# Kernel optimization log

Hardware: AMD Instinct MI355X
Metric: run time of the kernel (lower is better)

Reference implementation:

```python
import jax, jax.numpy as jnp
import numpy as np

B, N, C, H, W = 4, 5, 64, 100, 252  # N agents per sample (uniform record_len)


def setup_inputs() -> dict:
    key = jax.random.key(0)
    k1, k2, k3 = jax.random.split(key, 3)
    x = jax.random.normal(k1, (B * N, C, H, W), dtype=jnp.float32)
    rm = jax.random.normal(k2, (B * N, 2, H, W), dtype=jnp.float32)
    record_len = jnp.full((B,), N, dtype=jnp.int32)
    # normalized 2x3 affines (identity + small perturbation), shape (B, L, L, 2, 3)
    eye = jnp.broadcast_to(jnp.array([[1.0, 0.0, 0.0], [0.0, 1.0, 0.0]], jnp.float32), (B, N, N, 2, 3))
    pairwise_t_matrix = eye + 0.05 * jax.random.normal(k3, (B, N, N, 2, 3), dtype=jnp.float32)
    return {"x": x, "rm": rm, "record_len": record_len, "pairwise_t_matrix": pairwise_t_matrix}


def _warp_affine(feats, theta):
    # feats: (N, C, H, W), theta: (N, 2, 3). torch affine_grid + grid_sample,
    # bilinear, zeros padding, align_corners=False.
    xs = (2.0 * jnp.arange(W, dtype=jnp.float32) + 1.0) / W - 1.0
    ys = (2.0 * jnp.arange(H, dtype=jnp.float32) + 1.0) / H - 1.0
    gy, gx = jnp.meshgrid(ys, xs, indexing="ij")           # (H, W)
    base = jnp.stack([gx, gy, jnp.ones_like(gx)], axis=-1)  # (H, W, 3)
    coords = jnp.einsum("nij,hwj->nhwi", theta, base)       # (N, H, W, 2) normalized
    ix = ((coords[..., 0] + 1.0) * W - 1.0) * 0.5            # input pixel coords
    iy = ((coords[..., 1] + 1.0) * H - 1.0) * 0.5
    x0 = jnp.floor(ix); y0 = jnp.floor(iy)
    x1 = x0 + 1.0;      y1 = y0 + 1.0
    wx1 = ix - x0; wx0 = 1.0 - wx1
    wy1 = iy - y0; wy0 = 1.0 - wy1

    def gather(xi, yi):
        valid = (xi >= 0) & (xi <= W - 1) & (yi >= 0) & (yi <= H - 1)
        xc = jnp.clip(xi, 0, W - 1).astype(jnp.int32)
        yc = jnp.clip(yi, 0, H - 1).astype(jnp.int32)
        v = jax.vmap(lambda f, yy, xx: f[:, yy, xx])(feats, yc, xc)  # (N, C, H, W)
        return v * valid[:, None, :, :].astype(feats.dtype)

    out = (gather(x0, y0) * (wx0 * wy0)[:, None]
         + gather(x1, y0) * (wx1 * wy0)[:, None]
         + gather(x0, y1) * (wx0 * wy1)[:, None]
         + gather(x1, y1) * (wx1 * wy1)[:, None])
    return out  # (N, C, H, W)


def reference(x, rm, record_len, pairwise_t_matrix):
    # Where2commFusion, single-scale, MAX agg, communication disabled.
    # regroup: uniform record_len -> reshape (B, N, C, H, W)
    xr = x.reshape(B, N, C, H, W)
    theta = pairwise_t_matrix[:, 0, :, :, :]  # t_matrix[0, :N] per batch: (B, N, 2, 3)
    warped = jax.vmap(_warp_affine)(xr, theta)  # (B, N, C, H, W)
    x_fuse = jnp.max(warped, axis=1)            # (B, C, H, W)
    communication_rates = jnp.zeros((), dtype=jnp.float32)
    return (x_fuse, communication_rates)
```

## Files before the change

kernel.cpp:

```cpp
#include <hip/hip_runtime.h>
#include <math.h>

#define BB 4
#define NN 5
#define CC_DIM 64
#define HH 100
#define WW 252
#define HW (HH * WW)
#define CPT 8
#define NCHUNK (CC_DIM / CPT)

__global__ __launch_bounds__(256) void where2comm_fuse_kernel(
    const float* __restrict__ x,
    const float* __restrict__ ptm,
    float* __restrict__ out)
{
    const int idx = blockIdx.x * blockDim.x + threadIdx.x;
    const int total = BB * NCHUNK * HH * WW;
    if (idx >= total) {
        return;
    }

    int w = idx % WW;
    int t = idx / WW;
    int h = t % HH;
    t /= HH;
    int cc = t % NCHUNK;
    int b = t / NCHUNK;

    const float gx = (2.0f * (float)w + 1.0f) / (float)WW - 1.0f;
    const float gy = (2.0f * (float)h + 1.0f) / (float)HH - 1.0f;

    float acc[CPT];
#pragma unroll
    for (int c = 0; c < CPT; ++c) acc[c] = -INFINITY;

    const float* th_b = ptm + (size_t)b * (NN * NN * 6);

#pragma unroll
    for (int n = 0; n < NN; ++n) {
        const float t00 = th_b[n * 6 + 0];
        const float t01 = th_b[n * 6 + 1];
        const float t02 = th_b[n * 6 + 2];
        const float t10 = th_b[n * 6 + 3];
        const float t11 = th_b[n * 6 + 4];
        const float t12 = th_b[n * 6 + 5];

        const float cx = t00 * gx + t01 * gy + t02;
        const float cy = t10 * gx + t11 * gy + t12;

        const float ix = ((cx + 1.0f) * (float)WW - 1.0f) * 0.5f;
        const float iy = ((cy + 1.0f) * (float)HH - 1.0f) * 0.5f;

        const float x0f = floorf(ix);
        const float y0f = floorf(iy);
        const float x1f = x0f + 1.0f;
        const float y1f = y0f + 1.0f;

        const float wx1 = ix - x0f;
        const float wx0 = 1.0f - wx1;
        const float wy1 = iy - y0f;
        const float wy0 = 1.0f - wy1;

        const float mx0 = (x0f >= 0.0f && x0f <= (float)(WW - 1)) ? 1.0f : 0.0f;
        const float mx1 = (x1f >= 0.0f && x1f <= (float)(WW - 1)) ? 1.0f : 0.0f;
        const float my0 = (y0f >= 0.0f && y0f <= (float)(HH - 1)) ? 1.0f : 0.0f;
        const float my1 = (y1f >= 0.0f && y1f <= (float)(HH - 1)) ? 1.0f : 0.0f;

        const int xi0 = (int)fminf(fmaxf(x0f, 0.0f), (float)(WW - 1));
        const int xi1 = (int)fminf(fmaxf(x1f, 0.0f), (float)(WW - 1));
        const int yi0 = (int)fminf(fmaxf(y0f, 0.0f), (float)(HH - 1));
        const int yi1 = (int)fminf(fmaxf(y1f, 0.0f), (float)(HH - 1));

        const float e00 = wx0 * wy0 * mx0 * my0;
        const float e10 = wx1 * wy0 * mx1 * my0;
        const float e01 = wx0 * wy1 * mx0 * my1;
        const float e11 = wx1 * wy1 * mx1 * my1;

        const int o00 = yi0 * WW + xi0;
        const int o10 = yi0 * WW + xi1;
        const int o01 = yi1 * WW + xi0;
        const int o11 = yi1 * WW + xi1;

        const float* p = x + ((size_t)(b * NN + n) * CC_DIM + cc * CPT) * HW;

        float v00[CPT], v10[CPT], v01[CPT], v11[CPT];
#pragma unroll
        for (int c = 0; c < CPT; ++c) {
            const float* pc = p + (size_t)c * HW;
            v00[c] = pc[o00];
            v10[c] = pc[o10];
            v01[c] = pc[o01];
            v11[c] = pc[o11];
        }

#pragma unroll
        for (int c = 0; c < CPT; ++c) {
            float v = v00[c] * e00;
            v = fmaf(v10[c], e10, v);
            v = fmaf(v01[c], e01, v);
            v = fmaf(v11[c], e11, v);
            acc[c] = fmaxf(acc[c], v);
        }
    }

#pragma unroll
    for (int c = 0; c < CPT; ++c) {
        out[(((size_t)b * CC_DIM + cc * CPT + c) * HH + h) * WW + w] = acc[c];
    }

    if (idx == 0) {
        out[(size_t)BB * CC_DIM * HW] = 0.0f;
    }
}

extern "C" void kernel_launch(void* const* d_in, const int* in_sizes, int n_in,
                              void* d_out, int out_size, void* d_ws, size_t ws_size,
                              hipStream_t stream) {
    const float* x = (const float*)d_in[0];
    const float* ptm = (const float*)d_in[3];
    float* out = (float*)d_out;

    const int total = BB * NCHUNK * HH * WW;
    const int block = 256;
    const int grid = (total + block - 1) / block;
    where2comm_fuse_kernel<<<grid, block, 0, stream>>>(x, ptm, out);
}
```

Measured before the change: 58.02 us.

## Compute two output rows per thread and reuse shared bilinear source rows

Each thread now produces two adjacent output rows and loads each bilinear 2x2 window as two 8-byte row pairs from a clamped base, with clamping folded into the weights. When the second row's window matches or is one row below the first, the already-loaded source row is reused instead of reloaded. This aims to cut gather load count and per-pixel index math. It adds register pressure, divergent reuse branches and possibly unaligned vector loads.

```diff
diff --git a/kernel.cpp b/kernel.cpp
--- a/kernel.cpp
+++ b/kernel.cpp
@@ -9,6 +9,7 @@
 #define HW (HH * WW)
 #define CPT 8
 #define NCHUNK (CC_DIM / CPT)
+#define HP (HH / 2)
 
 __global__ __launch_bounds__(256) void where2comm_fuse_kernel(
     const float* __restrict__ x,
@@ -16,26 +17,26 @@
     float* __restrict__ out)
 {
     const int idx = blockIdx.x * blockDim.x + threadIdx.x;
-    const int total = BB * NCHUNK * HH * WW;
-    if (idx >= total) {
-        return;
-    }
 
     int w = idx % WW;
     int t = idx / WW;
-    int h = t % HH;
-    t /= HH;
+    int hp = t % HP;
+    t /= HP;
     int cc = t % NCHUNK;
     int b = t / NCHUNK;
 
+    const int h0 = 2 * hp;
+    const int h1 = h0 + 1;
+
     const float gx = (2.0f * (float)w + 1.0f) / (float)WW - 1.0f;
-    const float gy = (2.0f * (float)h + 1.0f) / (float)HH - 1.0f;
-
-    float acc[CPT];
-#pragma unroll
-    for (int c = 0; c < CPT; ++c) acc[c] = -INFINITY;
+    const float gy0 = (2.0f * (float)h0 + 1.0f) / (float)HH - 1.0f;
+    const float gy1 = (2.0f * (float)h1 + 1.0f) / (float)HH - 1.0f;
 
     const float* th_b = ptm + (size_t)b * (NN * NN * 6);
+
+    float acc0[CPT], acc1[CPT];
+#pragma unroll
+    for (int c = 0; c < CPT; ++c) { acc0[c] = -INFINITY; acc1[c] = -INFINITY; }
 
 #pragma unroll
     for (int n = 0; n < NN; ++n) {
@@ -46,67 +47,115 @@
         const float t11 = th_b[n * 6 + 4];
         const float t12 = th_b[n * 6 + 5];
 
-        const float cx = t00 * gx + t01 * gy + t02;
-        const float cy = t10 * gx + t11 * gy + t12;
+        int clA, rlA, clB, rlB;
+        float gA00, gA01, gA10, gA11, gB00, gB01, gB10, gB11;
 
-        const float ix = ((cx + 1.0f) * (float)WW - 1.0f) * 0.5f;
-        const float iy = ((cy + 1.0f) * (float)HH - 1.0f) * 0.5f;
+#define GEOM(GY, CL, RL, G00, G01, G10, G11)                                   \
+        {                                                                      \
+            const float cx = t00 * gx + t01 * (GY) + t02;                      \
+            const float cy = t10 * gx + t11 * (GY) + t12;                      \
+            const float ix = ((cx + 1.0f) * (float)WW - 1.0f) * 0.5f;          \
+            const float iy = ((cy + 1.0f) * (float)HH - 1.0f) * 0.5f;          \
+            const float x0f = floorf(ix);                                      \
+            const float y0f = floorf(iy);                                      \
+            const float x1f = x0f + 1.0f;                                      \
+            const float y1f = y0f + 1.0f;                                      \
+            const float wx1 = ix - x0f;                                        \
+            const float wx0 = 1.0f - wx1;                                      \
+            const float wy1 = iy - y0f;                                        \
+            const float wy0 = 1.0f - wy1;                                      \
+            const float mx0 = (x0f >= 0.0f && x0f <= (float)(WW - 1)) ? 1.0f : 0.0f; \
+            const float mx1 = (x1f >= 0.0f && x1f <= (float)(WW - 1)) ? 1.0f : 0.0f; \
+            const float my0 = (y0f >= 0.0f && y0f <= (float)(HH - 1)) ? 1.0f : 0.0f; \
+            const float my1 = (y1f >= 0.0f && y1f <= (float)(HH - 1)) ? 1.0f : 0.0f; \
+            const float e00 = wx0 * wy0 * mx0 * my0;                           \
+            const float e10 = wx1 * wy0 * mx1 * my0;                           \
+            const float e01 = wx0 * wy1 * mx0 * my1;                           \
+            const float e11 = wx1 * wy1 * mx1 * my1;                           \
+            const int xi0 = (int)fminf(fmaxf(x0f, 0.0f), (float)(WW - 1));     \
+            const int xi1 = (int)fminf(fmaxf(x1f, 0.0f), (float)(WW - 1));     \
+            const int yi0 = (int)fminf(fmaxf(y0f, 0.0f), (float)(HH - 1));     \
+            const int yi1 = (int)fminf(fmaxf(y1f, 0.0f), (float)(HH - 1));     \
+            CL = (int)fminf(fmaxf(x0f, 0.0f), (float)(WW - 2));                \
+            RL = (int)fminf(fmaxf(y0f, 0.0f), (float)(HH - 2));                \
+            const float sx0 = (float)(xi0 - CL);                               \
+            const float sx1 = (float)(xi1 - CL);                               \
+            const float sy0 = (float)(yi0 - RL);                               \
+            const float sy1 = (float)(yi1 - RL);                               \
+            const float nx0 = 1.0f - sx0, nx1 = 1.0f - sx1;                    \
+            const float ny0 = 1.0f - sy0, ny1 = 1.0f - sy1;                    \
+            G00 = e00 * nx0 * ny0 + e10 * nx1 * ny0 + e01 * nx0 * ny1 + e11 * nx1 * ny1; \
+            G01 = e00 * sx0 * ny0 + e10 * sx1 * ny0 + e01 * sx0 * ny1 + e11 * sx1 * ny1; \
+            G10 = e00 * nx0 * sy0 + e10 * nx1 * sy0 + e01 * nx0 * sy1 + e11 * nx1 * sy1; \
+            G11 = e00 * sx0 * sy0 + e10 * sx1 * sy0 + e01 * sx0 * sy1 + e11 * sx1 * sy1; \
+        }
 
-        const float x0f = floorf(ix);
-        const float y0f = floorf(iy);
-        const float x1f = x0f + 1.0f;
-        const float y1f = y0f + 1.0f;
+        GEOM(gy0, clA, rlA, gA00, gA01, gA10, gA11)
+        GEOM(gy1, clB, rlB, gB00, gB01, gB10, gB11)
+#undef GEOM
 
-        const float wx1 = ix - x0f;
-        const float wx0 = 1.0f - wx1;
-        const float wy1 = iy - y0f;
-        const float wy0 = 1.0f - wy1;
+        const float* plane = x + ((size_t)(b * NN + n) * CC_DIM + cc * CPT) * HW;
+        const int offA = rlA * WW + clA;
+        const int offB = rlB * WW + clB;
 
-        const float mx0 = (x0f >= 0.0f && x0f <= (float)(WW - 1)) ? 1.0f : 0.0f;
-        const float mx1 = (x1f >= 0.0f && x1f <= (float)(WW - 1)) ? 1.0f : 0.0f;
-        const float my0 = (y0f >= 0.0f && y0f <= (float)(HH - 1)) ? 1.0f : 0.0f;
-        const float my1 = (y1f >= 0.0f && y1f <= (float)(HH - 1)) ? 1.0f : 0.0f;
-
-        const int xi0 = (int)fminf(fmaxf(x0f, 0.0f), (float)(WW - 1));
-        const int xi1 = (int)fminf(fmaxf(x1f, 0.0f), (float)(WW - 1));
-        const int yi0 = (int)fminf(fmaxf(y0f, 0.0f), (float)(HH - 1));
-        const int yi1 = (int)fminf(fmaxf(y1f, 0.0f), (float)(HH - 1));
-
-        const float e00 = wx0 * wy0 * mx0 * my0;
-        const float e10 = wx1 * wy0 * mx1 * my0;
-        const float e01 = wx0 * wy1 * mx0 * my1;
-        const float e11 = wx1 * wy1 * mx1 * my1;
-
-        const int o00 = yi0 * WW + xi0;
-        const int o10 = yi0 * WW + xi1;
-        const int o01 = yi1 * WW + xi0;
-        const int o11 = yi1 * WW + xi1;
-
-        const float* p = x + ((size_t)(b * NN + n) * CC_DIM + cc * CPT) * HW;
-
-        float v00[CPT], v10[CPT], v01[CPT], v11[CPT];
+        float L0[CPT][2], L1[CPT][2];
 #pragma unroll
         for (int c = 0; c < CPT; ++c) {
-            const float* pc = p + (size_t)c * HW;
-            v00[c] = pc[o00];
-            v10[c] = pc[o10];
-            v01[c] = pc[o01];
-            v11[c] = pc[o11];
+            const float* pc = plane + (size_t)c * HW + offA;
+            __builtin_memcpy(&L0[c][0], pc, 8);
+            __builtin_memcpy(&L1[c][0], pc + WW, 8);
         }
 
 #pragma unroll
         for (int c = 0; c < CPT; ++c) {
-            float v = v00[c] * e00;
-            v = fmaf(v10[c], e10, v);
-            v = fmaf(v01[c], e01, v);
-            v = fmaf(v11[c], e11, v);
-            acc[c] = fmaxf(acc[c], v);
+            float v = L0[c][0] * gA00;
+            v = fmaf(L0[c][1], gA01, v);
+            v = fmaf(L1[c][0], gA10, v);
+            v = fmaf(L1[c][1], gA11, v);
+            acc0[c] = fmaxf(acc0[c], v);
+        }
+
+        const bool sameCol = (clB == clA);
+        const bool reuse0 = sameCol && (rlB == rlA);
+        const bool reuse1 = sameCol && (rlB == rlA + 1);
+
+        float P[CPT][2], Q[CPT][2];
+        if (reuse0) {
+#pragma unroll
+            for (int c = 0; c < CPT; ++c) {
+                P[c][0] = L0[c][0]; P[c][1] = L0[c][1];
+                Q[c][0] = L1[c][0]; Q[c][1] = L1[c][1];
+            }
+        } else if (reuse1) {
+#pragma unroll
+            for (int c = 0; c < CPT; ++c) {
+                P[c][0] = L1[c][0]; P[c][1] = L1[c][1];
+                __builtin_memcpy(&Q[c][0], plane + (size_t)c * HW + offB + WW, 8);
+            }
+        } else {
+#pragma unroll
+            for (int c = 0; c < CPT; ++c) {
+                const float* pc = plane + (size_t)c * HW + offB;
+                __builtin_memcpy(&P[c][0], pc, 8);
+                __builtin_memcpy(&Q[c][0], pc + WW, 8);
+            }
+        }
+
+#pragma unroll
+        for (int c = 0; c < CPT; ++c) {
+            float v = P[c][0] * gB00;
+            v = fmaf(P[c][1], gB01, v);
+            v = fmaf(Q[c][0], gB10, v);
+            v = fmaf(Q[c][1], gB11, v);
+            acc1[c] = fmaxf(acc1[c], v);
         }
     }
 
 #pragma unroll
     for (int c = 0; c < CPT; ++c) {
-        out[(((size_t)b * CC_DIM + cc * CPT + c) * HH + h) * WW + w] = acc[c];
+        const size_t rowbase = ((size_t)(b * CC_DIM + cc * CPT + c) * HH + h0) * WW + w;
+        out[rowbase] = acc0[c];
+        out[rowbase + WW] = acc1[c];
     }
 
     if (idx == 0) {
@@ -121,8 +170,8 @@
     const float* ptm = (const float*)d_in[3];
     float* out = (float*)d_out;
 
-    const int total = BB * NCHUNK * HH * WW;
+    const int total = BB * NCHUNK * HP * WW;
     const int block = 256;
-    const int grid = (total + block - 1) / block;
+    const int grid = total / block;
     where2comm_fuse_kernel<<<grid, block, 0, stream>>>(x, ptm, out);
 }
```

After: 80.47 us. 1.39x slower.
